# Optimization experiments

Measured on AMD Instinct MI355X. Metric: run time of the kernel, lower is better.

## Reference

```python
import jax, jax.numpy as jnp
import numpy as np

NUM_HEADS = 16
DIM_MODEL = 1024
DIM_K = DIM_MODEL // NUM_HEADS
B, S = 2, 2048


def _linear_params(key, d_in, d_out):
    kw, kb = jax.random.split(key)
    bound = 1.0 / np.sqrt(d_in)
    W = jax.random.uniform(kw, (d_out, d_in), jnp.float32, -bound, bound)
    b = jax.random.uniform(kb, (d_out,), jnp.float32, -bound, bound)
    return W, b


def setup_inputs() -> dict:
    key = jax.random.key(0)
    ks = jax.random.split(key, 7)
    Q_in = jax.random.normal(ks[0], (B, S, DIM_MODEL), jnp.float32)
    K_in = jax.random.normal(ks[1], (B, S, DIM_MODEL), jnp.float32)
    V_in = jax.random.normal(ks[2], (B, S, DIM_MODEL), jnp.float32)
    Wq, bq = _linear_params(ks[3], DIM_MODEL, DIM_MODEL)
    Wk, bk = _linear_params(ks[4], DIM_MODEL, DIM_MODEL)
    Wv, bv = _linear_params(ks[5], DIM_MODEL, DIM_MODEL)
    Wo, bo = _linear_params(ks[6], DIM_MODEL, DIM_MODEL)
    return {"Q_in": Q_in, "K_in": K_in, "V_in": V_in,
            "Wq": Wq, "bq": bq, "Wk": Wk, "bk": bk,
            "Wv": Wv, "bv": bv, "Wo": Wo, "bo": bo}


def reference(Q_in, K_in, V_in, Wq, bq, Wk, bk, Wv, bv, Wo, bo):
    # QKV projections (nn.Linear: x @ W.T + b)
    Q = Q_in @ Wq.T + bq
    K = K_in @ Wk.T + bk
    V = V_in @ Wv.T + bv
    # [B, S, D] -> [B, H, S, dk]
    def split_heads(x):
        return x.reshape(B, S, NUM_HEADS, DIM_K).transpose(0, 2, 1, 3)
    Qh, Kh, Vh = split_heads(Q), split_heads(K), split_heads(V)
    # Scaled dot-product attention
    scale = 1.0 / np.sqrt(DIM_K)
    scores = jnp.einsum('bhqd,bhkd->bhqk', Qh, Kh) * scale  # [B,H,S,S]
    attn = jax.nn.softmax(scores, axis=-1)
    out = jnp.einsum('bhqk,bhkd->bhqd', attn, Vh)  # [B,H,S,dk]
    # Merge heads -> [B, S, D]
    out = out.transpose(0, 2, 1, 3).reshape(B, S, DIM_MODEL)
    return out @ Wo.T + bo
```

## Files before the change

### kernel.cpp

```cpp
#include <hip/hip_runtime.h>
#include <stdint.h>

#define BB 2
#define SS 2048
#define DD 1024
#define HH 16
#define DKK 64
#define MT (BB*SS)

#define GSTRIDE 40
#define ASTRIDE 72

using short8  = __attribute__((ext_vector_type(8))) short;
using floatx4 = __attribute__((ext_vector_type(4))) float;
using u16x4   = __attribute__((ext_vector_type(4))) unsigned short;
typedef unsigned short u16;

__device__ __forceinline__ u16 f2b(float f) {
  union { float f; unsigned u; } v; v.f = f;
  return (u16)((v.u + 0x7FFFu + ((v.u >> 16) & 1u)) >> 16);
}
__device__ __forceinline__ void pack16(const float4* p, short8& lo, short8& hi) {
  float4 x0 = p[0], x1 = p[1], x2 = p[2], x3 = p[3];
  lo[0]=(short)f2b(x0.x); lo[1]=(short)f2b(x0.y); lo[2]=(short)f2b(x0.z); lo[3]=(short)f2b(x0.w);
  lo[4]=(short)f2b(x1.x); lo[5]=(short)f2b(x1.y); lo[6]=(short)f2b(x1.z); lo[7]=(short)f2b(x1.w);
  hi[0]=(short)f2b(x2.x); hi[1]=(short)f2b(x2.y); hi[2]=(short)f2b(x2.z); hi[3]=(short)f2b(x2.w);
  hi[4]=(short)f2b(x3.x); hi[5]=(short)f2b(x3.y); hi[6]=(short)f2b(x3.z); hi[7]=(short)f2b(x3.w);
}
__device__ __forceinline__ void gload16(const u16* g, u16* l) {
  __builtin_amdgcn_global_load_lds(
      (const __attribute__((address_space(1))) void*)g,
      (__attribute__((address_space(3))) void*)l, 16, 0, 0);
}

__global__ __launch_bounds__(256) void cast_all(
    const float* __restrict__ Qin, const float* __restrict__ Kin,
    const float* __restrict__ Vin, const float* __restrict__ Wq,
    const float* __restrict__ Wk,  const float* __restrict__ Wv,
    const float* __restrict__ Wo,
    u16* __restrict__ cQ, u16* __restrict__ cK, u16* __restrict__ cV,
    u16* __restrict__ cWq, u16* __restrict__ cWk, u16* __restrict__ cWv,
    u16* __restrict__ cWo)
{
  const int y = blockIdx.y;
  if (y >= 3 && blockIdx.x >= (DD*DD/8/256)) return;
  const float* s; u16* d;
  switch (y) {
    case 0: s = Qin; d = cQ;  break;
    case 1: s = Kin; d = cK;  break;
    case 2: s = Vin; d = cV;  break;
    case 3: s = Wq;  d = cWq; break;
    case 4: s = Wk;  d = cWk; break;
    case 5: s = Wv;  d = cWv; break;
    default: s = Wo; d = cWo; break;
  }
  const size_t g = (size_t)blockIdx.x * 256 + threadIdx.x;
  float4 x0 = ((const float4*)s)[g*2], x1 = ((const float4*)s)[g*2+1];
  short8 lo;
  lo[0]=(short)f2b(x0.x); lo[1]=(short)f2b(x0.y); lo[2]=(short)f2b(x0.z); lo[3]=(short)f2b(x0.w);
  lo[4]=(short)f2b(x1.x); lo[5]=(short)f2b(x1.y); lo[6]=(short)f2b(x1.z); lo[7]=(short)f2b(x1.w);
  ((short8*)d)[g] = lo;
}
__global__ __launch_bounds__(256) void cast_w3(
    const float* __restrict__ w0, const float* __restrict__ w1,
    const float* __restrict__ w2, u16* __restrict__ o)
{
  const float* s = (blockIdx.y == 0) ? w0 : (blockIdx.y == 1) ? w1 : w2;
  u16* d = o + (size_t)blockIdx.y * (DD * DD);
  const size_t g = (size_t)blockIdx.x * 256 + threadIdx.x;
  float4 x0 = ((const float4*)s)[g*2], x1 = ((const float4*)s)[g*2+1];
  short8 lo;
  lo[0]=(short)f2b(x0.x); lo[1]=(short)f2b(x0.y); lo[2]=(short)f2b(x0.z); lo[3]=(short)f2b(x0.w);
  lo[4]=(short)f2b(x1.x); lo[5]=(short)f2b(x1.y); lo[6]=(short)f2b(x1.z); lo[7]=(short)f2b(x1.w);
  ((short8*)d)[g] = lo;
}

template<bool OUT_F32>
__device__ __forceinline__ void gemm_async(
    const u16* __restrict__ A, const u16* __restrict__ W,
    const float* __restrict__ bias, void* __restrict__ Cv,
    const int K, const int N, const int m0, const int n0, const float scale)
{
  __shared__ __align__(16) u16 sA[128*64];
  __shared__ __align__(16) u16 sB[128*64];

  const int tid  = threadIdx.x;
  const int wave = tid >> 6;
  const int lane = tid & 63;
  const int quad = lane >> 4;
  const int lr   = lane & 15;
  const int wm   = wave >> 1;
  const int wn   = wave & 1;
  const int srow = lane >> 3;
  const int swz  = (((lane & 7) ^ ((srow & 1) << 2)) << 3);

  floatx4 acc[4][4];
#pragma unroll
  for (int i = 0; i < 4; ++i)
#pragma unroll
    for (int j = 0; j < 4; ++j) acc[i][j] = (floatx4){0.f, 0.f, 0.f, 0.f};

  const u16* pA[4]; const u16* pW[4];
#pragma unroll
  for (int c = 0; c < 4; ++c) {
    const int row = (wave + c*4) * 8 + srow;
    pA[c] = A + (size_t)(m0 + row) * K + swz;
    pW[c] = W + (size_t)(n0 + row) * K + swz;
  }

  const int nk = K >> 6;
  for (int kt = 0; kt < nk; ++kt) {
    const int k0 = kt << 6;
#pragma unroll
    for (int c = 0; c < 4; ++c) {
      gload16(pA[c] + k0, sA + (wave + c*4) * 512);
      gload16(pW[c] + k0, sB + (wave + c*4) * 512);
    }
    __syncthreads();

#pragma unroll
    for (int h2 = 0; h2 < 2; ++h2) {
      const int csel = (quad << 3) + ((h2 ^ (lr & 1)) << 5);
      short8 af[4], bf[4];
#pragma unroll
      for (int t = 0; t < 4; ++t) {
        af[t] = *(const short8*)(sA + (wm*64 + t*16 + lr)*64 + csel);
        bf[t] = *(const short8*)(sB + (wn*64 + t*16 + lr)*64 + csel);
      }
#pragma unroll
      for (int i = 0; i < 4; ++i)
#pragma unroll
        for (int j = 0; j < 4; ++j)
          acc[i][j] = __builtin_amdgcn_mfma_f32_16x16x32_bf16(af[i], bf[j], acc[i][j], 0, 0, 0);
    }
    __syncthreads();
  }

#pragma unroll
  for (int i = 0; i < 4; ++i) {
    const int mb = m0 + wm*64 + i*16 + quad*4;
#pragma unroll
    for (int j = 0; j < 4; ++j) {
      const int n = n0 + wn*64 + j*16 + lr;
      const float bsv = bias[n];
#pragma unroll
      for (int r = 0; r < 4; ++r) {
        const size_t idx = (size_t)(mb + r) * N + n;
        const float v = (acc[i][j][r] + bsv) * scale;
        if (OUT_F32) ((float*)Cv)[idx] = v;
        else         ((u16*)Cv)[idx]   = f2b(v);
      }
    }
  }
}

__global__ __launch_bounds__(256, 3) void gemm_qkv_async(
    const u16* __restrict__ cQ, const u16* __restrict__ cK, const u16* __restrict__ cV,
    const u16* __restrict__ cWq, const u16* __restrict__ cWk, const u16* __restrict__ cWv,
    const float* __restrict__ bq, const float* __restrict__ bk, const float* __restrict__ bv,
    u16* __restrict__ oQ, u16* __restrict__ oK, u16* __restrict__ oV)
{
  const int wsel = blockIdx.x >> 3;
  const int n0 = (blockIdx.x & 7) * 128;
  const int m0 = blockIdx.y * 128;
  const u16* A; const u16* W; const float* bias; u16* C;
  if (wsel == 0)      { A = cQ; W = cWq; bias = bq; C = oQ; }
  else if (wsel == 1) { A = cK; W = cWk; bias = bk; C = oK; }
  else                { A = cV; W = cWv; bias = bv; C = oV; }
  const float scale = (wsel == 0) ? 0.125f : 1.0f;
  gemm_async<false>(A, W, bias, C, DD, DD, m0, n0, scale);
}

__global__ __launch_bounds__(256, 3) void gemm_out_async(
    const u16* __restrict__ A, const u16* __restrict__ cWo,
    const float* __restrict__ bias, float* __restrict__ C)
{
  gemm_async<true>(A, cWo, bias, C, DD, DD, blockIdx.y * 128, blockIdx.x * 128, 1.0f);
}

template<bool A_BF16, bool W_BF16, bool OUT_F32>
__device__ __forceinline__ void gemm_core(
    const void* __restrict__ A, const void* __restrict__ W,
    const float* __restrict__ bias, void* __restrict__ Cv,
    const int K, const int N, const int m0, const int n0, const float scale)
{
  __shared__ __align__(16) u16 sA[128*GSTRIDE];
  __shared__ __align__(16) u16 sB[128*GSTRIDE];

  const int tid  = threadIdx.x;
  const int wave = tid >> 6;
  const int lane = tid & 63;
  const int quad = lane >> 4;
  const int lr   = lane & 15;
  const int wm   = wave >> 1;
  const int wn   = wave & 1;
  const int srow = tid >> 1;
  const int scol = (tid & 1) * 16;

  floatx4 acc[4][4];
#pragma unroll
  for (int i = 0; i < 4; ++i)
#pragma unroll
    for (int j = 0; j < 4; ++j) acc[i][j] = (floatx4){0.f, 0.f, 0.f, 0.f};

  const size_t offA = (size_t)(m0 + srow) * K + scol;
  const size_t offW = (size_t)(n0 + srow) * K + scol;

  const int nk = K >> 5;
  for (int kt = 0; kt < nk; ++kt) {
    const int k0 = kt << 5;
    short8 a0, a1, b0, b1;
    if (A_BF16) {
      const u16* p = (const u16*)A + offA + k0;
      a0 = *(const short8*)p; a1 = *(const short8*)(p + 8);
    } else {
      pack16((const float4*)((const float*)A + offA + k0), a0, a1);
    }
    if (W_BF16) {
      const u16* p = (const u16*)W + offW + k0;
      b0 = *(const short8*)p; b1 = *(const short8*)(p + 8);
    } else {
      pack16((const float4*)((const float*)W + offW + k0), b0, b1);
    }
    __syncthreads();
    *(short8*)(sA + srow * GSTRIDE + scol)     = a0;
    *(short8*)(sA + srow * GSTRIDE + scol + 8) = a1;
    *(short8*)(sB + srow * GSTRIDE + scol)     = b0;
    *(short8*)(sB + srow * GSTRIDE + scol + 8) = b1;
    __syncthreads();

    short8 af[4], bf[4];
#pragma unroll
    for (int t = 0; t < 4; ++t) {
      af[t] = *(const short8*)(sA + (wm*64 + t*16 + lr)*GSTRIDE + quad*8);
      bf[t] = *(const short8*)(sB + (wn*64 + t*16 + lr)*GSTRIDE + quad*8);
    }
#pragma unroll
    for (int i = 0; i < 4; ++i)
#pragma unroll
      for (int j = 0; j < 4; ++j)
        acc[i][j] = __builtin_amdgcn_mfma_f32_16x16x32_bf16(af[i], bf[j], acc[i][j], 0, 0, 0);
  }

#pragma unroll
  for (int i = 0; i < 4; ++i) {
    const int mb = m0 + wm*64 + i*16 + quad*4;
#pragma unroll
    for (int j = 0; j < 4; ++j) {
      const int n = n0 + wn*64 + j*16 + lr;
      const float bsv = bias[n];
#pragma unroll
      for (int r = 0; r < 4; ++r) {
        const size_t idx = (size_t)(mb + r) * N + n;
        const float v = (acc[i][j][r] + bsv) * scale;
        if (OUT_F32) ((float*)Cv)[idx] = v;
        else         ((u16*)Cv)[idx]   = f2b(v);
      }
    }
  }
}

__global__ __launch_bounds__(256, 2) void gemm_qkv_fb(
    const float* __restrict__ Qin, const float* __restrict__ Kin, const float* __restrict__ Vin,
    const u16* __restrict__ cWq, const u16* __restrict__ cWk, const u16* __restrict__ cWv,
    const float* __restrict__ bq, const float* __restrict__ bk, const float* __restrict__ bv,
    u16* __restrict__ oQ, u16* __restrict__ oK, u16* __restrict__ oV)
{
  const int wsel = blockIdx.x >> 3;
  const int n0 = (blockIdx.x & 7) * 128;
  const int m0 = blockIdx.y * 128;
  const float* A; const u16* W; const float* bias; u16* C;
  if (wsel == 0)      { A = Qin; W = cWq; bias = bq; C = oQ; }
  else if (wsel == 1) { A = Kin; W = cWk; bias = bk; C = oK; }
  else                { A = Vin; W = cWv; bias = bv; C = oV; }
  const float scale = (wsel == 0) ? 0.125f : 1.0f;
  gemm_core<false, true, false>(A, W, bias, C, DD, DD, m0, n0, scale);
}
__global__ __launch_bounds__(256, 2) void gemm_out_fb(
    const u16* __restrict__ A, const float* __restrict__ W,
    const float* __restrict__ bias, float* __restrict__ C)
{
  gemm_core<true, false, true>((const void*)A, (const void*)W, bias, C, DD, DD,
                               blockIdx.y * 128, blockIdx.x * 128, 1.0f);
}

__global__ __launch_bounds__(256) void transpose_v(
    const u16* __restrict__ Vp, u16* __restrict__ Vt)
{
  __shared__ u16 t[64 * 65];
  const int st = blockIdx.x, h = blockIdx.y, b = blockIdx.z;

  const int r  = threadIdx.x >> 2;
  const int c0 = (threadIdx.x & 3) * 16;
  const u16* src = Vp + ((size_t)(b * SS + st * 64 + r)) * DD + h * 64 + c0;
  short8 v0 = *(const short8*)src;
  short8 v1 = *(const short8*)(src + 8);
#pragma unroll
  for (int i = 0; i < 8; ++i) {
    t[r * 65 + c0 + i]     = (u16)v0[i];
    t[r * 65 + c0 + 8 + i] = (u16)v1[i];
  }
  __syncthreads();
  union { u16 a[16]; short8 v[2]; } ob;
#pragma unroll
  for (int i = 0; i < 16; ++i) ob.a[i] = t[(c0 + i) * 65 + r];
  u16* dst = Vt + (((size_t)(b * HH + h)) * DKK + r) * SS + st * 64 + c0;
  *(short8*)dst       = ob.v[0];
  *(short8*)(dst + 8) = ob.v[1];
}

__global__ __launch_bounds__(512, 4) void attn(
    const u16* __restrict__ Qp, const u16* __restrict__ Kp,
    const u16* __restrict__ Vt, u16* __restrict__ O)
{
  __shared__ __align__(16) u16 sK[64 * ASTRIDE];
  __shared__ __align__(16) u16 sV[64 * ASTRIDE];
  __shared__ __align__(16) u16 sP[8][16 * ASTRIDE];

  const int tid = threadIdx.x, wave = tid >> 6, lane = tid & 63;
  const int quad = lane >> 4, lr = lane & 15;

  const int flat = (blockIdx.z * 16 + blockIdx.y) * 16 + blockIdx.x;
  const int swzb = (flat & 7) * 64 + (flat >> 3);
  const int qb = swzb & 15;
  const int h  = (swzb >> 4) & 15;
  const int b  = swzb >> 8;
  const size_t vbase = ((size_t)(b * HH + h)) * DKK * SS;

  short8 qf0, qf1;
  {
    const u16* qr = Qp + ((size_t)(b * SS + qb * 128 + wave * 16 + lr)) * DD + h * 64 + quad * 8;
    qf0 = *(const short8*)qr;
    qf1 = *(const short8*)(qr + 32);
  }

  floatx4 accO[4];
  float m_l = -3e38f, l_l = 0.f;
#pragma unroll
  for (int t = 0; t < 4; ++t) accO[t] = (floatx4){0.f, 0.f, 0.f, 0.f};

  const int sr = tid >> 3, sc = (tid & 7) * 8;
  const u16* kg = Kp + ((size_t)(b * SS + sr)) * DD + h * 64 + sc;
  const u16* vg = Vt + vbase + (size_t)sr * SS + sc;
  u16* dk = sK + sr * ASTRIDE + sc;
  u16* dv = sV + sr * ASTRIDE + sc;

  for (int kt = 0; kt < SS / 64; ++kt) {
    __syncthreads();
    *(short8*)dk = *(const short8*)(kg + (size_t)(kt * 64) * DD);
    *(short8*)dv = *(const short8*)(vg + kt * 64);
    __syncthreads();

    floatx4 st[4];
#pragma unroll
    for (int t = 0; t < 4; ++t) {
      short8 ka0 = *(const short8*)(sK + (t*16 + lr) * ASTRIDE + quad * 8);
      short8 ka1 = *(const short8*)(sK + (t*16 + lr) * ASTRIDE + 32 + quad * 8);
      floatx4 cc = (floatx4){0.f, 0.f, 0.f, 0.f};
      cc = __builtin_amdgcn_mfma_f32_16x16x32_bf16(ka0, qf0, cc, 0, 0, 0);
      cc = __builtin_amdgcn_mfma_f32_16x16x32_bf16(ka1, qf1, cc, 0, 0, 0);
      st[t] = cc;
    }

    float mx = st[0][0];
#pragma unroll
    for (int t = 0; t < 4; ++t)
#pragma unroll
      for (int r = 0; r < 4; ++r) mx = fmaxf(mx, st[t][r]);
    mx = fmaxf(mx, __shfl_xor(mx, 16, 64));
    mx = fmaxf(mx, __shfl_xor(mx, 32, 64));
    const float mn = fmaxf(m_l, mx);
    const float al = __expf(m_l - mn);
    m_l = mn;
    float rs = 0.f;
    u16x4 pk[4];
#pragma unroll
    for (int t = 0; t < 4; ++t)
#pragma unroll
      for (int r = 0; r < 4; ++r) {
        const float p = __expf(st[t][r] - mn);
        rs += p;
        pk[t][r] = f2b(p);
      }
    rs += __shfl_xor(rs, 16, 64);
    rs += __shfl_xor(rs, 32, 64);
    l_l = l_l * al + rs;

    float arow[4];
#pragma unroll
    for (int r = 0; r < 4; ++r) arow[r] = __shfl(al, quad * 4 + r, 64);
#pragma unroll
    for (int t = 0; t < 4; ++t) {
      floatx4 o = accO[t];
      o[0] *= arow[0]; o[1] *= arow[1]; o[2] *= arow[2]; o[3] *= arow[3];
      accO[t] = o;
    }
#pragma unroll
    for (int t = 0; t < 4; ++t)
      *(u16x4*)(sP[wave] + lr * ASTRIDE + t * 16 + quad * 4) = pk[t];

    short8 p0 = *(const short8*)(sP[wave] + lr * ASTRIDE + quad * 8);
    short8 p1 = *(const short8*)(sP[wave] + lr * ASTRIDE + 32 + quad * 8);
#pragma unroll
    for (int t = 0; t < 4; ++t) {
      short8 v0 = *(const short8*)(sV + (t*16 + lr) * ASTRIDE + quad * 8);
      short8 v1 = *(const short8*)(sV + (t*16 + lr) * ASTRIDE + 32 + quad * 8);
      accO[t] = __builtin_amdgcn_mfma_f32_16x16x32_bf16(p0, v0, accO[t], 0, 0, 0);
      accO[t] = __builtin_amdgcn_mfma_f32_16x16x32_bf16(p1, v1, accO[t], 0, 0, 0);
    }
  }

  {
    float lrow[4];
#pragma unroll
    for (int r = 0; r < 4; ++r) lrow[r] = __shfl(l_l, quad * 4 + r, 64);
#pragma unroll
    for (int t = 0; t < 4; ++t)
#pragma unroll
      for (int r = 0; r < 4; ++r) {
        const int s = qb * 128 + wave * 16 + quad * 4 + r;
        const int d = h * 64 + t * 16 + lr;
        O[((size_t)(b * SS + s)) * DD + d] = f2b(accO[t][r] / lrow[r]);
      }
  }
}

extern "C" void kernel_launch(void* const* d_in, const int* in_sizes, int n_in,
                              void* d_out, int out_size, void* d_ws, size_t ws_size,
                              hipStream_t stream)
{
  const float* Qin = (const float*)d_in[0];
  const float* Kin = (const float*)d_in[1];
  const float* Vin = (const float*)d_in[2];
  const float* Wq  = (const float*)d_in[3];
  const float* bq  = (const float*)d_in[4];
  const float* Wk  = (const float*)d_in[5];
  const float* bk  = (const float*)d_in[6];
  const float* Wv  = (const float*)d_in[7];
  const float* bv  = (const float*)d_in[8];
  const float* Wo  = (const float*)d_in[9];
  const float* bo  = (const float*)d_in[10];
  float* out = (float*)d_out;

  const size_t TSZ = (size_t)MT * DD;
  const size_t WSZ = (size_t)DD * DD;
  dim3 blk(256);

  u16* cWq = (u16*)d_out;
  u16* cWk = cWq + WSZ;
  u16* cWv = cWk + WSZ;

  u16* pQ   = (u16*)d_ws;
  u16* pK   = pQ  + TSZ;
  u16* pV   = pK  + TSZ;
  u16* wsVt = pV  + TSZ;
  u16* wsO  = wsVt + TSZ;

  if (ws_size >= (8*TSZ + WSZ) * sizeof(u16)) {
    u16* cQ  = wsO + TSZ;
    u16* cK  = cQ  + TSZ;
    u16* cV  = cK  + TSZ;
    u16* cWo = cV  + TSZ;
    cast_all<<<dim3(TSZ/8/256, 7), blk, 0, stream>>>(
        Qin, Kin, Vin, Wq, Wk, Wv, Wo, cQ, cK, cV, cWq, cWk, cWv, cWo);
    gemm_qkv_async<<<dim3(24, MT/128), blk, 0, stream>>>(
        cQ, cK, cV, cWq, cWk, cWv, bq, bk, bv, pQ, pK, pV);
    transpose_v<<<dim3(SS/64, HH, BB), blk, 0, stream>>>(pV, wsVt);
    attn<<<dim3(SS/128, HH, BB), dim3(512), 0, stream>>>(pQ, pK, wsVt, wsO);
    gemm_out_async<<<dim3(DD/128, MT/128), blk, 0, stream>>>(wsO, cWo, bo, out);
  } else {
    cast_w3<<<dim3(WSZ/8/256, 3), blk, 0, stream>>>(Wq, Wk, Wv, cWq);
    gemm_qkv_fb<<<dim3(24, MT/128), blk, 0, stream>>>(
        Qin, Kin, Vin, cWq, cWk, cWv, bq, bk, bv, pQ, pK, pV);
    transpose_v<<<dim3(SS/64, HH, BB), blk, 0, stream>>>(pV, wsVt);
    attn<<<dim3(SS/128, HH, BB), dim3(512), 0, stream>>>(pQ, pK, wsVt, wsO);
    gemm_out_fb<<<dim3(DD/128, MT/128), blk, 0, stream>>>(wsO, Wo, bo, out);
  }
}
```

Baseline: 258.2 us.

## Double-buffer K/V tiles in attention with register prefetch and single barrier

Splits the shared K and V tiles into two buffers and prefetches the next tile from global memory into registers while the current tile is computed. The loop now needs one barrier per iteration instead of two, and global load latency can overlap the MFMA work. In exchange it doubles K/V shared memory and uses more registers, which may reduce occupancy at 512 threads with launch bounds of 4 blocks.

```diff
diff --git a/kernel.cpp b/kernel.cpp
--- a/kernel.cpp
+++ b/kernel.cpp
@@ -313,8 +313,8 @@
     const u16* __restrict__ Qp, const u16* __restrict__ Kp,
     const u16* __restrict__ Vt, u16* __restrict__ O)
 {
-  __shared__ __align__(16) u16 sK[64 * ASTRIDE];
-  __shared__ __align__(16) u16 sV[64 * ASTRIDE];
+  __shared__ __align__(16) u16 sK[2][64 * ASTRIDE];
+  __shared__ __align__(16) u16 sV[2][64 * ASTRIDE];
   __shared__ __align__(16) u16 sP[8][16 * ASTRIDE];
 
   const int tid = threadIdx.x, wave = tid >> 6, lane = tid & 63;
@@ -340,22 +340,39 @@
   for (int t = 0; t < 4; ++t) accO[t] = (floatx4){0.f, 0.f, 0.f, 0.f};
 
   const int sr = tid >> 3, sc = (tid & 7) * 8;
-  const u16* kg = Kp + ((size_t)(b * SS + sr)) * DD + h * 64 + sc;
-  const u16* vg = Vt + vbase + (size_t)sr * SS + sc;
-  u16* dk = sK + sr * ASTRIDE + sc;
-  u16* dv = sV + sr * ASTRIDE + sc;
+  const u16* kp = Kp + ((size_t)(b * SS + sr)) * DD + h * 64 + sc;
+  const u16* vp = Vt + vbase + (size_t)sr * SS + sc;
+  u16* dkb[2] = { sK[0] + sr * ASTRIDE + sc, sK[1] + sr * ASTRIDE + sc };
+  u16* dvb[2] = { sV[0] + sr * ASTRIDE + sc, sV[1] + sr * ASTRIDE + sc };
+
+  short8 rk = *(const short8*)kp;
+  short8 rv = *(const short8*)vp;
+  *(short8*)dkb[0] = rk;
+  *(short8*)dvb[0] = rv;
+  kp += (size_t)64 * DD; vp += 64;
+  rk = *(const short8*)kp;
+  rv = *(const short8*)vp;
+  __syncthreads();
 
   for (int kt = 0; kt < SS / 64; ++kt) {
-    __syncthreads();
-    *(short8*)dk = *(const short8*)(kg + (size_t)(kt * 64) * DD);
-    *(short8*)dv = *(const short8*)(vg + kt * 64);
-    __syncthreads();
+    const int cur = kt & 1;
+    if (kt < SS / 64 - 1) {
+      *(short8*)dkb[cur ^ 1] = rk;
+      *(short8*)dvb[cur ^ 1] = rv;
+    }
+    if (kt < SS / 64 - 2) {
+      kp += (size_t)64 * DD; vp += 64;
+      rk = *(const short8*)kp;
+      rv = *(const short8*)vp;
+    }
+    const u16* sKc = sK[cur];
+    const u16* sVc = sV[cur];
 
     floatx4 st[4];
 #pragma unroll
     for (int t = 0; t < 4; ++t) {
-      short8 ka0 = *(const short8*)(sK + (t*16 + lr) * ASTRIDE + quad * 8);
-      short8 ka1 = *(const short8*)(sK + (t*16 + lr) * ASTRIDE + 32 + quad * 8);
+      short8 ka0 = *(const short8*)(sKc + (t*16 + lr) * ASTRIDE + quad * 8);
+      short8 ka1 = *(const short8*)(sKc + (t*16 + lr) * ASTRIDE + 32 + quad * 8);
       floatx4 cc = (floatx4){0.f, 0.f, 0.f, 0.f};
       cc = __builtin_amdgcn_mfma_f32_16x16x32_bf16(ka0, qf0, cc, 0, 0, 0);
       cc = __builtin_amdgcn_mfma_f32_16x16x32_bf16(ka1, qf1, cc, 0, 0, 0);
@@ -403,11 +420,13 @@
     short8 p1 = *(const short8*)(sP[wave] + lr * ASTRIDE + 32 + quad * 8);
 #pragma unroll
     for (int t = 0; t < 4; ++t) {
-      short8 v0 = *(const short8*)(sV + (t*16 + lr) * ASTRIDE + quad * 8);
-      short8 v1 = *(const short8*)(sV + (t*16 + lr) * ASTRIDE + 32 + quad * 8);
+      short8 v0 = *(const short8*)(sVc + (t*16 + lr) * ASTRIDE + quad * 8);
+      short8 v1 = *(const short8*)(sVc + (t*16 + lr) * ASTRIDE + 32 + quad * 8);
       accO[t] = __builtin_amdgcn_mfma_f32_16x16x32_bf16(p0, v0, accO[t], 0, 0, 0);
       accO[t] = __builtin_amdgcn_mfma_f32_16x16x32_bf16(p1, v1, accO[t], 0, 0, 0);
     }
+
+    __syncthreads();
   }
 
   {
```

After: 257.2 us. About the same (-0.4%).
